# Kernel optimization log

Measured on AMD Instinct MI355X. Metric: run time of the kernel, lower is better.

## Reference

```python
import jax, jax.numpy as jnp
import numpy as np

N_NODES = 20000
N_EDGES = 320000
EMB = 256
K_DIFF = 3
BN_EPS = 1e-5


def conv1d(x, w, b, stride):
    # x: [N, Cin, L], w: [Cout, Cin, K]
    y = jax.lax.conv_general_dilated(x, w, window_strides=(stride,), padding='VALID',
                                     dimension_numbers=('NCH', 'OIH', 'NCH'))
    return y + b[None, :, None]


def batchnorm_train(x, gamma, beta):
    # training-mode BatchNorm1d over (N, L) per channel, biased variance
    m = jnp.mean(x, axis=(0, 2), keepdims=True)
    v = jnp.var(x, axis=(0, 2), keepdims=True)
    return (x - m) * jax.lax.rsqrt(v + BN_EPS) * gamma[None, :, None] + beta[None, :, None]


def dconv(X, W, b, row, col, norm_out, norm_in, n):
    # Diffusion convolution (pytorch_geometric_temporal DConv), K hops,
    # forward (out-degree) and backward (in-degree) random walks.
    def prop(x, norm):
        msg = norm[:, None] * x[row]                    # [E, F] gather
        return jax.ops.segment_sum(msg, col, num_segments=n)  # scatter-add to targets

    K = W.shape[1]
    Tx_0 = X
    Tx_1 = X
    H = X @ W[0, 0] + X @ W[1, 0]
    if K > 1:
        Tx_1_o = prop(X, norm_out)
        Tx_1_i = prop(X, norm_in)
        H = H + Tx_1_o @ W[0, 1] + Tx_1_i @ W[1, 1]
    for k in range(2, K):
        Tx_2_o = 2.0 * prop(Tx_1_o, norm_out) - Tx_0
        Tx_2_i = 2.0 * prop(Tx_1_i, norm_in) - Tx_0
        H = H + Tx_2_o @ W[0, k] + Tx_2_i @ W[1, k]
        Tx_0, Tx_1_o, Tx_1_i = Tx_1, Tx_2_o, Tx_2_i
    return H + b


def setup_inputs() -> dict:
    key = jax.random.key(0)
    ks = jax.random.split(key, 16)
    d_in = 2 * EMB  # concat([X, H])
    inp = {
        'x': jax.random.normal(ks[0], (N_NODES, 1, 100), dtype=jnp.float32),
        'edge_index': jax.random.randint(ks[1], (2, N_EDGES), 0, N_NODES, dtype=jnp.int32),
        'hidden_state': jax.random.normal(ks[2], (N_NODES, EMB), dtype=jnp.float32),
        'conv1_w': jax.random.normal(ks[3], (32, 1, 10), dtype=jnp.float32) * 0.2,
        'conv1_b': jnp.zeros((32,), jnp.float32),
        'bn1_gamma': jnp.ones((32,), jnp.float32),
        'bn1_beta': jnp.zeros((32,), jnp.float32),
        'conv2_w': jax.random.normal(ks[4], (32, 32, 10), dtype=jnp.float32) * 0.05,
        'conv2_b': jnp.zeros((32,), jnp.float32),
        'bn2_gamma': jnp.ones((32,), jnp.float32),
        'bn2_beta': jnp.zeros((32,), jnp.float32),
        'W_z': jax.random.normal(ks[5], (2, K_DIFF, d_in, EMB), dtype=jnp.float32) * 0.05,
        'b_z': jnp.zeros((EMB,), jnp.float32),
        'W_r': jax.random.normal(ks[6], (2, K_DIFF, d_in, EMB), dtype=jnp.float32) * 0.05,
        'b_r': jnp.zeros((EMB,), jnp.float32),
        'W_h': jax.random.normal(ks[7], (2, K_DIFF, d_in, EMB), dtype=jnp.float32) * 0.05,
        'b_h': jnp.zeros((EMB,), jnp.float32),
    }
    return inp


def reference(x, edge_index, hidden_state, conv1_w, conv1_b, bn1_gamma, bn1_beta,
              conv2_w, conv2_b, bn2_gamma, bn2_beta, W_z, b_z, W_r, b_r, W_h, b_h):
    n = x.shape[0]
    # CNN embedding: conv -> relu -> bn, twice
    h = batchnorm_train(jax.nn.relu(conv1d(x, conv1_w, conv1_b, 3)), bn1_gamma, bn1_beta)
    h = batchnorm_train(jax.nn.relu(conv1d(h, conv2_w, conv2_b, 3)), bn2_gamma, bn2_beta)
    X = h.reshape(n, -1)  # [N, EMB]

    row, col = edge_index[0], edge_index[1]
    ones = jnp.ones((row.shape[0],), X.dtype)
    deg_out = jax.ops.segment_sum(ones, row, num_segments=n)
    deg_in = jax.ops.segment_sum(ones, col, num_segments=n)
    norm_out = (1.0 / deg_out)[row]
    norm_in = (1.0 / deg_in)[col]

    H0 = hidden_state
    XH = jnp.concatenate([X, H0], axis=1)
    Z = jax.nn.sigmoid(dconv(XH, W_z, b_z, row, col, norm_out, norm_in, n))
    R = jax.nn.sigmoid(dconv(XH, W_r, b_r, row, col, norm_out, norm_in, n))
    XRH = jnp.concatenate([X, R * H0], axis=1)
    H_tilde = jnp.tanh(dconv(XRH, W_h, b_h, row, col, norm_out, norm_in, n))
    H = Z * H0 + (1.0 - Z) * H_tilde
    return jax.nn.relu(H)
```

## Files before the change

kernel.cpp:

```cpp
#include <hip/hip_runtime.h>
#include <cstdint>
#include <cstddef>

#define NN 20000
#define NE 320000
#define SBUF 10240000

typedef float f32x4 __attribute__((ext_vector_type(4)));
typedef short s16x8 __attribute__((ext_vector_type(8)));
typedef unsigned short us;

__device__ __forceinline__ us f2bf(float x){
    unsigned u = __float_as_uint(x);
    unsigned r = (u + 0x7fffu + ((u >> 16) & 1u)) >> 16;
    return (us)r;
}
__device__ __forceinline__ float bf2f(us s){
    return __uint_as_float(((unsigned)s) << 16);
}

__device__ __forceinline__ void gl16(const void* g, void* l){
    __builtin_amdgcn_global_load_lds((const __attribute__((address_space(1))) unsigned int*)g,
                                     (__attribute__((address_space(3))) unsigned int*)l, 16, 0, 0);
}

__device__ __forceinline__ void upd8(uint4 v, float w, float* ao, float* ai){
    float f0=__uint_as_float(v.x<<16), f1=__uint_as_float(v.x&0xffff0000u);
    float f2=__uint_as_float(v.y<<16), f3=__uint_as_float(v.y&0xffff0000u);
    float f4=__uint_as_float(v.z<<16), f5=__uint_as_float(v.z&0xffff0000u);
    float f6=__uint_as_float(v.w<<16), f7=__uint_as_float(v.w&0xffff0000u);
    ao[0]=fmaf(w,f0,ao[0]); ao[1]=fmaf(w,f1,ao[1]); ao[2]=fmaf(w,f2,ao[2]); ao[3]=fmaf(w,f3,ao[3]);
    ao[4]=fmaf(w,f4,ao[4]); ao[5]=fmaf(w,f5,ao[5]); ao[6]=fmaf(w,f6,ao[6]); ao[7]=fmaf(w,f7,ao[7]);
    ai[0]+=f0; ai[1]+=f1; ai[2]+=f2; ai[3]+=f3; ai[4]+=f4; ai[5]+=f5; ai[6]+=f6; ai[7]+=f7;
}
__device__ __forceinline__ void updw(uint4 v, float w, float* a){
    float f0=__uint_as_float(v.x<<16), f1=__uint_as_float(v.x&0xffff0000u);
    float f2=__uint_as_float(v.y<<16), f3=__uint_as_float(v.y&0xffff0000u);
    float f4=__uint_as_float(v.z<<16), f5=__uint_as_float(v.z&0xffff0000u);
    float f6=__uint_as_float(v.w<<16), f7=__uint_as_float(v.w&0xffff0000u);
    a[0]=fmaf(w,f0,a[0]); a[1]=fmaf(w,f1,a[1]); a[2]=fmaf(w,f2,a[2]); a[3]=fmaf(w,f3,a[3]);
    a[4]=fmaf(w,f4,a[4]); a[5]=fmaf(w,f5,a[5]); a[6]=fmaf(w,f6,a[6]); a[7]=fmaf(w,f7,a[7]);
}
__device__ __forceinline__ uint4 pack8(const float* a){
    uint4 r;
    r.x=((unsigned)f2bf(a[1])<<16)|f2bf(a[0]);
    r.y=((unsigned)f2bf(a[3])<<16)|f2bf(a[2]);
    r.z=((unsigned)f2bf(a[5])<<16)|f2bf(a[4]);
    r.w=((unsigned)f2bf(a[7])<<16)|f2bf(a[6]);
    return r;
}
__device__ __forceinline__ uint4 pack8s(const float* a, float s){
    uint4 r;
    r.x=((unsigned)f2bf(s*a[1])<<16)|f2bf(s*a[0]);
    r.y=((unsigned)f2bf(s*a[3])<<16)|f2bf(s*a[2]);
    r.z=((unsigned)f2bf(s*a[5])<<16)|f2bf(s*a[4]);
    r.w=((unsigned)f2bf(s*a[7])<<16)|f2bf(s*a[6]);
    return r;
}


__global__ void k_zero(uint32_t* p, int n){
    int i = blockIdx.x*256 + threadIdx.x;
    if(i < n) p[i] = 0u;
}

__global__ void k_degree(const int* __restrict__ ei, int* degout, int* degin){
    int e = blockIdx.x*256 + threadIdx.x;
    if(e < NE){
        atomicAdd(&degout[ei[e]], 1);
        atomicAdd(&degin[ei[NE+e]], 1);
    }
}

__global__ void k_scan(const int* __restrict__ degin, int* __restrict__ coloff,
                       float* __restrict__ invdegin){
    __shared__ int part[1024];
    int t = threadIdx.x;
    int base = t*20;
    int s = 0;
    for(int k=0;k<20;k++){ int i = base+k; if(i < NN) s += degin[i]; }
    part[t] = s;
    __syncthreads();
    for(int off=1; off<1024; off<<=1){
        int v = (t>=off) ? part[t-off] : 0;
        __syncthreads();
        part[t] += v;
        __syncthreads();
    }
    int run = (t>0) ? part[t-1] : 0;
    for(int k=0;k<20;k++){
        int i = base+k;
        if(i < NN){
            int d = degin[i];
            coloff[i] = run;
            run += d;
            invdegin[i] = (d>0) ? (1.0f/(float)d) : 0.0f;
        }
    }
    if(t==1023) coloff[NN] = part[1023];
}

__global__ void k_csr(const int* __restrict__ ei, const int* __restrict__ degout,
                      const int* __restrict__ coloff, int* cnt, int2* __restrict__ ew){
    int e = blockIdx.x*256 + threadIdx.x;
    if(e < NE){
        int r = ei[e], c = ei[NE+e];
        int pos = coloff[c] + atomicAdd(&cnt[c], 1);
        int2 v; v.x = r; v.y = __float_as_int(1.0f/(float)degout[r]);
        ew[pos] = v;
    }
}


__global__ void k_conv1(const float* __restrict__ x, const float* __restrict__ w1,
                        const float* __restrict__ b1, us* __restrict__ y1b){
    __shared__ float w[320];
    __shared__ float bb[32];
    int t = threadIdx.x;
    for(int i=t;i<320;i+=256) w[i] = w1[i];
    if(t < 32) bb[t] = b1[t];
    __syncthreads();
    int gid = blockIdx.x*256 + t;
    if(gid >= NN*31) return;
    int node = gid/31, p = gid - node*31;
    const float* xr = x + node*100 + 3*p;
    float xv[10];
    #pragma unroll
    for(int k=0;k<10;k++) xv[k] = xr[k];
    us* yo = y1b + (size_t)node*1024 + p;
    #pragma unroll
    for(int c=0;c<32;c++){
        float a = bb[c];
        #pragma unroll
        for(int k=0;k<10;k++) a = fmaf(w[c*10+k], xv[k], a);
        yo[c*32] = f2bf(fmaxf(a, 0.0f));
    }
    if(p == 0){
        #pragma unroll
        for(int c=0;c<32;c++) y1b[(size_t)node*1024 + c*32 + 31] = 0;
    }
}

template<int SLOTS, int PPC>
__global__ void k_chanstats_bf(const us* __restrict__ y, float* __restrict__ sq){
    int tid = blockIdx.x*blockDim.x + threadIdx.x;
    int slot = tid & (SLOTS-1);
    int node0 = tid / SLOTS;
    int nstride = (gridDim.x*blockDim.x) / SLOTS;
    int c = slot / PPC;
    float s = 0.f, q = 0.f;
    for(int n=node0; n<NN; n+=nstride){
        float v = bf2f(y[(size_t)n*SLOTS + slot]);
        s += v; q = fmaf(v, v, q);
    }
    #pragma unroll
    for(int m=PPC>>1; m>0; m>>=1){
        s += __shfl_xor(s, m);
        q += __shfl_xor(q, m);
    }
    if((threadIdx.x & (PPC-1)) == 0){
        atomicAdd(&sq[c], s);
        atomicAdd(&sq[32+c], q);
    }
}

__global__ void k_bnfin(const float* __restrict__ sq, const float* __restrict__ gamma,
                        const float* __restrict__ beta, float* __restrict__ scsh,
                        float inv_count){
    int c = threadIdx.x;
    if(c < 32){
        float m = sq[c]*inv_count;
        float v = sq[32+c]*inv_count - m*m;
        float sc = gamma[c]*rsqrtf(v + 1e-5f);
        scsh[c] = sc;
        scsh[32+c] = beta[c] - m*sc;
    }
}

__global__ void __launch_bounds__(256) k_conv2(const us* __restrict__ y1b,
                        const float* __restrict__ w2, const float* __restrict__ b2,
                        const float* __restrict__ scsh1, us* __restrict__ Xpre){
    __shared__ float wlds[10240];
    __shared__ float hlds[8*1040];
    int t = threadIdx.x;
    int node0 = blockIdx.x*8;
    #pragma unroll
    for(int j=0;j<40;j++){
        int idx = j*256 + t;
        int ck = idx>>5, c2 = idx&31;
        wlds[ck*32 + c2] = w2[c2*320 + ck];
    }
    #pragma unroll
    for(int j=0;j<32;j++){
        int idx = j*256 + t;
        int nl = idx>>10, i = idx&1023;
        int c = i>>5;
        hlds[nl*1040 + i] = fmaf(scsh1[c], bf2f(y1b[(size_t)(node0+nl)*1024 + i]), scsh1[32+c]);
    }
    __syncthreads();
    int nl = t>>5, c2 = t&31;
    int hbase = nl*1040;
    float acc[8];
    float b = b2[c2];
    #pragma unroll
    for(int p=0;p<8;p++) acc[p] = b;
    for(int c=0;c<32;c++){
        float wr[10];
        #pragma unroll
        for(int k=0;k<10;k++) wr[k] = wlds[(c*10+k)*32 + c2];
        float hv[32];
        #pragma unroll
        for(int q=0;q<8;q++){
            float4 v = *(const float4*)&hlds[hbase + c*32 + q*4];
            hv[q*4+0]=v.x; hv[q*4+1]=v.y; hv[q*4+2]=v.z; hv[q*4+3]=v.w;
        }
        #pragma unroll
        for(int p=0;p<8;p++){
            #pragma unroll
            for(int k=0;k<10;k++)
                acc[p] = fmaf(wr[k], hv[3*p+k], acc[p]);
        }
    }
    uint4 pk;
    pk.x = ((unsigned)f2bf(fmaxf(acc[1],0.f))<<16) | f2bf(fmaxf(acc[0],0.f));
    pk.y = ((unsigned)f2bf(fmaxf(acc[3],0.f))<<16) | f2bf(fmaxf(acc[2],0.f));
    pk.z = ((unsigned)f2bf(fmaxf(acc[5],0.f))<<16) | f2bf(fmaxf(acc[4],0.f));
    pk.w = ((unsigned)f2bf(fmaxf(acc[7],0.f))<<16) | f2bf(fmaxf(acc[6],0.f));
    *(uint4*)&Xpre[(size_t)(node0+nl)*256 + c2*8] = pk;
}

__global__ void __launch_bounds__(256) k_prep(const us* __restrict__ Xpre,
        const float* __restrict__ scsh, const float* __restrict__ h0,
        us* __restrict__ XHp){
    int node = blockIdx.x*4 + (threadIdx.x>>6);
    if(node >= NN) return;
    int lane = threadIdx.x & 63;
    int half = lane>>5, g = lane&31;
    uint4 o;
    if(half == 0){
        uint4 v = *(const uint4*)(Xpre + (size_t)node*256 + g*8);
        float sc = scsh[g], sh = scsh[32+g];
        float y[8];
        y[0]=fmaf(sc,__uint_as_float(v.x<<16),sh); y[1]=fmaf(sc,__uint_as_float(v.x&0xffff0000u),sh);
        y[2]=fmaf(sc,__uint_as_float(v.y<<16),sh); y[3]=fmaf(sc,__uint_as_float(v.y&0xffff0000u),sh);
        y[4]=fmaf(sc,__uint_as_float(v.z<<16),sh); y[5]=fmaf(sc,__uint_as_float(v.z&0xffff0000u),sh);
        y[6]=fmaf(sc,__uint_as_float(v.w<<16),sh); y[7]=fmaf(sc,__uint_as_float(v.w&0xffff0000u),sh);
        o = pack8(y);
    }else{
        float4 a = *(const float4*)(h0 + (size_t)node*256 + g*8);
        float4 b = *(const float4*)(h0 + (size_t)node*256 + g*8 + 4);
        float y[8] = {a.x,a.y,a.z,a.w,b.x,b.y,b.z,b.w};
        o = pack8(y);
    }
    *(uint4*)(XHp + (size_t)node*512 + (size_t)g*16 + half*8) = o;
}


__device__ __forceinline__ float weff_val(const float* W, int term, size_t base){
    const size_t S = 512*256;
    if(term==0)      return W[0*S+base] + W[3*S+base] - W[2*S+base] - W[5*S+base];
    else if(term==1) return W[1*S+base];
    else if(term==2) return W[4*S+base];
    else if(term==3) return 2.0f*W[2*S+base];
    else             return 2.0f*W[5*S+base];
}

__global__ void k_weff_zr_t(const float* __restrict__ Wz, const float* __restrict__ Wr,
                            us* __restrict__ Wt){
    int k = blockIdx.x*256 + threadIdx.x;
    int col = blockIdx.y;
    const float* W = (col < 256) ? Wz : Wr;
    int j = col & 255;
    int kb = k >> 8, rr = k & 255;
    size_t base = (size_t)((kb & 1)*256 + rr)*256 + j;
    Wt[(size_t)col*2560 + k] = f2bf(weff_val(W, kb>>1, base));
}

__global__ void k_weff_h_t(const float* __restrict__ Wh, us* __restrict__ Wt){
    int k = blockIdx.x*256 + threadIdx.x;
    int col = blockIdx.y;
    int kb = k >> 8, rr = k & 255;
    size_t base = (size_t)((kb & 1)*256 + rr)*256 + col;
    Wt[(size_t)col*2560 + k] = f2bf(weff_val(Wh, kb>>1, base));
}


__global__ void __launch_bounds__(256) k_prop1(const us* __restrict__ XHp,
        const int* __restrict__ coloff, const int2* __restrict__ ew,
        const float* __restrict__ invdeg, us* __restrict__ T1op, us* __restrict__ T1ip){
    int node = blockIdx.x*4 + (threadIdx.x>>6);
    if(node >= NN) return;
    int lane = threadIdx.x & 63;
    size_t lo = (size_t)(lane&31)*16 + (lane>>5)*8;
    int s = coloff[node], e = coloff[node+1];
    float ao[8]={0,0,0,0,0,0,0,0}, ai[8]={0,0,0,0,0,0,0,0};
    int j = s;
    for(; j+7 < e; j += 8){
        int2 ed[8]; uint4 v[8];
        #pragma unroll
        for(int i=0;i<8;i++) ed[i] = ew[j+i];
        #pragma unroll
        for(int i=0;i<8;i++) v[i] = *(const uint4*)(XHp+(size_t)ed[i].x*512+lo);
        #pragma unroll
        for(int i=0;i<8;i++) upd8(v[i], __int_as_float(ed[i].y), ao, ai);
    }
    for(; j < e; j++){
        int2 ed = ew[j];
        uint4 v = *(const uint4*)(XHp+(size_t)ed.x*512+lo);
        upd8(v, __int_as_float(ed.y), ao, ai);
    }
    float wi = invdeg[node];
    *(uint4*)(T1op+(size_t)node*512+lo) = pack8(ao);
    *(uint4*)(T1ip+(size_t)node*512+lo) = pack8s(ai,wi);
}

__global__ void __launch_bounds__(256) k_prop2(const us* __restrict__ T1op,
        const us* __restrict__ T1ip,
        const int* __restrict__ coloff, const int2* __restrict__ ew,
        const float* __restrict__ invdeg, us* __restrict__ P2op, us* __restrict__ P2ip){
    int node = blockIdx.x*4 + (threadIdx.x>>6);
    if(node >= NN) return;
    int lane = threadIdx.x & 63;
    size_t lo = (size_t)(lane&31)*16 + (lane>>5)*8;
    int s = coloff[node], e = coloff[node+1];
    float ao[8]={0,0,0,0,0,0,0,0}, ai[8]={0,0,0,0,0,0,0,0};
    int j = s;
    for(; j+3 < e; j += 4){
        int2 ed[4]; uint4 va[4], vb[4];
        #pragma unroll
        for(int i=0;i<4;i++) ed[i] = ew[j+i];
        #pragma unroll
        for(int i=0;i<4;i++){
            size_t o = (size_t)ed[i].x*512+lo;
            va[i] = *(const uint4*)(T1op+o);
            vb[i] = *(const uint4*)(T1ip+o);
        }
        #pragma unroll
        for(int i=0;i<4;i++){
            updw(va[i], __int_as_float(ed[i].y), ao);
            updw(vb[i], 1.0f, ai);
        }
    }
    for(; j < e; j++){
        int2 ed = ew[j];
        size_t o = (size_t)ed.x*512+lo;
        updw(*(const uint4*)(T1op+o), __int_as_float(ed.y), ao);
        updw(*(const uint4*)(T1ip+o), 1.0f, ai);
    }
    float wi = invdeg[node];
    *(uint4*)(P2op+(size_t)node*512+lo) = pack8(ao);
    *(uint4*)(P2ip+(size_t)node*512+lo) = pack8s(ai,wi);
}

__global__ void __launch_bounds__(256) k_propu(const us* __restrict__ Yin,
        const int* __restrict__ coloff, const int2* __restrict__ ew,
        const float* __restrict__ invdeg, us* __restrict__ Pout){
    int node = blockIdx.x*4 + (threadIdx.x>>6);
    if(node >= NN) return;
    int lane = threadIdx.x & 63;
    int half = lane>>5;
    size_t lo = (size_t)(lane&31)*16 + half*8;
    int s = coloff[node], e = coloff[node+1];
    float a[8]={0,0,0,0,0,0,0,0};
    int j = s;
    for(; j+7 < e; j += 8){
        int2 ed[8]; uint4 v[8];
        #pragma unroll
        for(int i=0;i<8;i++) ed[i] = ew[j+i];
        #pragma unroll
        for(int i=0;i<8;i++) v[i] = *(const uint4*)(Yin+(size_t)ed[i].x*512+lo);
        #pragma unroll
        for(int i=0;i<8;i++) updw(v[i], half ? 1.0f : __int_as_float(ed[i].y), a);
    }
    for(; j < e; j++){
        int2 ed = ew[j];
        uint4 v = *(const uint4*)(Yin+(size_t)ed.x*512+lo);
        updw(v, half ? 1.0f : __int_as_float(ed.y), a);
    }
    float sc = half ? invdeg[node] : 1.0f;
    *(uint4*)(Pout+(size_t)node*512+lo) = pack8s(a,sc);
}


template<int MODE, int BNT>
__global__ void __launch_bounds__(256) k_gemm(const us* __restrict__ XG,
        const us* __restrict__ RG, const us* __restrict__ Wt,
        const float* __restrict__ bias0, const float* __restrict__ bias1,
        const float* __restrict__ h0, const float* __restrict__ Zin,
        float* __restrict__ out0, us* __restrict__ out1){
    constexpr int WN = BNT/32;
    constexpr int NB = BNT/64;
    __shared__ us As[2][4096];
    __shared__ us Bs[2][BNT*32];
    int t = threadIdx.x;
    int wid = t >> 6, lane = t & 63;
    int l15 = lane & 15, kg = lane >> 4;

    int bid = blockIdx.x;
    int xcd = bid & 7, sblk = bid >> 3;
    int cidx = sblk & 3, r = (sblk >> 2)*8 + xcd;
    if(r >= 157) return;
    int row0 = r*128, col0 = cidx*BNT;
    int rowbase = (wid >> 1)*64, colbase = (wid & 1)*(BNT/2);
    int swz = (l15 >> 1) & 3;

    int srA[2], sgA[2];
    size_t rowoffA[2];
    #pragma unroll
    for(int i=0;i<2;i++){
        int c = t + i*256;
        srA[i] = c >> 2;
        sgA[i] = (c & 3) ^ ((srA[i] >> 1) & 3);
        int gr = row0 + srA[i];
        gr = (gr < NN) ? gr : NN-1;
        rowoffA[i] = (size_t)gr*512 + (size_t)sgA[i]*16;
    }
    int srB[NB], sgB[NB];
    size_t coloffB[NB];
    #pragma unroll
    for(int i=0;i<NB;i++){
        int c = t + i*256;
        srB[i] = c >> 2;
        sgB[i] = (c & 3) ^ ((srB[i] >> 1) & 3);
        coloffB[i] = (size_t)(col0+srB[i])*2560 + (size_t)sgB[i]*8;
    }

    f32x4 acc[4][WN] = {};

    auto stage = [&](int buf, int s){
        int kb = s >> 3;
        int ktc = (s & 7) * 4;
        const us* Ap;
        if(MODE == 0){
            Ap = XG + (size_t)(kb >> 1) * SBUF + (size_t)(kb & 1) * 8;
        }else{
            if((kb & 1) == 0) Ap = XG + (size_t)(kb >> 1) * SBUF;
            else Ap = RG + (size_t)((kb + 1) >> 2) * SBUF + (size_t)(((kb + 1) >> 1) & 1) * 8;
        }
        #pragma unroll
        for(int i=0;i<2;i++)
            gl16(Ap + rowoffA[i] + (size_t)ktc*16, &As[buf][(t+i*256)*8]);
        const us* Wp = Wt + (size_t)kb*256 + (s & 7)*32;
        #pragma unroll
        for(int i=0;i<NB;i++)
            gl16(Wp + coloffB[i], &Bs[buf][(t+i*256)*8]);
    };

    stage(0, 0);
    stage(1, 1);
    for(int step=0; step<80; ++step){
        int cur = step & 1;
        if(step < 79){
            if(MODE == 0) asm volatile("s_waitcnt vmcnt(4)" ::: "memory");
            else          asm volatile("s_waitcnt vmcnt(3)" ::: "memory");
        }else{
            asm volatile("s_waitcnt vmcnt(0)" ::: "memory");
        }
        __builtin_amdgcn_s_barrier();
        s16x8 af[4], bfr[WN];
        #pragma unroll
        for(int i=0;i<4;i++){
            int row = rowbase + i*16 + l15;
            af[i] = *(const s16x8*)&As[cur][(row*4 + (kg ^ swz))*8];
        }
        #pragma unroll
        for(int n=0;n<WN;n++){
            int colr = colbase + n*16 + l15;
            bfr[n] = *(const s16x8*)&Bs[cur][(colr*4 + (kg ^ swz))*8];
        }
        asm volatile("s_waitcnt lgkmcnt(0)" ::: "memory");
        __builtin_amdgcn_sched_barrier(0);
        __builtin_amdgcn_s_barrier();
        if(step < 78) stage(cur, step+2);
        __builtin_amdgcn_s_setprio(1);
        #pragma unroll
        for(int mi=0;mi<4;mi++){
            #pragma unroll
            for(int ni=0;ni<WN;ni++){
                acc[mi][ni] = __builtin_amdgcn_mfma_f32_16x16x32_bf16(
                    af[mi], bfr[ni], acc[mi][ni], 0, 0, 0);
            }
        }
        __builtin_amdgcn_s_setprio(0);
    }

    #pragma unroll
    for(int mi=0;mi<4;mi++){
        int gr0 = row0 + rowbase + mi*16 + kg*4;
        #pragma unroll
        for(int ni=0;ni<WN;ni++){
            int j = col0 + colbase + ni*16 + l15;
            #pragma unroll
            for(int rr=0;rr<4;rr++){
                int gr = gr0 + rr;
                if(gr < NN){
                    float a = acc[mi][ni][rr];
                    if(MODE == 0){
                        if(j < 256){
                            out0[(size_t)gr*256 + j] = 1.0f/(1.0f + expf(-(a + bias0[j])));
                        }else{
                            int jj = j - 256;
                            float rv = 1.0f/(1.0f + expf(-(a + bias1[jj])));
                            us v = f2bf(rv * h0[(size_t)gr*256 + jj]);
                            size_t base = (size_t)gr*512 + (size_t)(jj>>3)*16 + (jj&7);
                            out1[base] = v;
                            out1[base+8] = v;
                        }
                    }else{
                        float z = Zin[(size_t)gr*256 + j];
                        float ht = tanhf(a + bias0[j]);
                        float H = z*h0[(size_t)gr*256 + j] + (1.0f - z)*ht;
                        out0[(size_t)gr*256 + j] = fmaxf(H, 0.0f);
                    }
                }
            }
        }
    }
}


extern "C" void kernel_launch(void* const* d_in, const int* in_sizes, int n_in,
                              void* d_out, int out_size, void* d_ws, size_t ws_size,
                              hipStream_t stream){
    const float* x   = (const float*)d_in[0];
    const int*   ei  = (const int*)  d_in[1];
    const float* h0  = (const float*)d_in[2];
    const float* w1  = (const float*)d_in[3];
    const float* b1  = (const float*)d_in[4];
    const float* g1  = (const float*)d_in[5];
    const float* be1 = (const float*)d_in[6];
    const float* w2  = (const float*)d_in[7];
    const float* b2  = (const float*)d_in[8];
    const float* g2  = (const float*)d_in[9];
    const float* be2 = (const float*)d_in[10];
    const float* Wz  = (const float*)d_in[11];
    const float* bz  = (const float*)d_in[12];
    const float* Wr  = (const float*)d_in[13];
    const float* br  = (const float*)d_in[14];
    const float* Wh  = (const float*)d_in[15];
    const float* bh  = (const float*)d_in[16];
    float* out = (float*)d_out;
    float* wsf = (float*)d_ws;
    (void)in_sizes; (void)n_in; (void)out_size;

    const size_t O_DEGO=0, O_DEGI=20000, O_CNT=40000, O_BN=60000;
    const size_t O_COLOFF=60288, O_EW=80384, O_INVDEG=720384;
    const size_t O_WTZR=740480, O_WTH=1395840;
    const size_t O_XPRE=1723520;
    const size_t O_XG=4283520;
    const size_t O_RG=29883520;
    const size_t O_Z=45243520;
    const size_t WS_NEED_BYTES = (size_t)50363520 * 4;
    if(ws_size < WS_NEED_BYTES) return;

    const size_t SW = 5120000;

    int* degout = (int*)(wsf + O_DEGO);
    int* degin  = (int*)(wsf + O_DEGI);
    int* cnt    = (int*)(wsf + O_CNT);
    float* bn   = wsf + O_BN;
    int* coloff = (int*)(wsf + O_COLOFF);
    int2* ew    = (int2*)(wsf + O_EW);
    float* invdeg = wsf + O_INVDEG;
    us* Wtzr = (us*)(wsf + O_WTZR);
    us* Wth  = (us*)(wsf + O_WTH);
    us* Xpre = (us*)(wsf + O_XPRE);
    us* XG   = (us*)(wsf + O_XG);
    us* RG   = (us*)(wsf + O_RG);
    us* XHp  = XG;
    us* T1op = (us*)(wsf + O_XG + SW);
    us* T1ip = (us*)(wsf + O_XG + 2*SW);
    us* P2op = (us*)(wsf + O_XG + 3*SW);
    us* P2ip = (us*)(wsf + O_XG + 4*SW);
    us* RHp  = RG;
    us* Q1p  = (us*)(wsf + O_RG + SW);
    us* Q2p  = (us*)(wsf + O_RG + 2*SW);
    float* Z = wsf + O_Z;
    us* y1b  = T1op;

    k_zero<<<236,256,0,stream>>>((uint32_t*)(wsf + O_DEGO), 60256);
    k_degree<<<1250,256,0,stream>>>(ei, degout, degin);
    k_scan<<<1,1024,0,stream>>>(degin, coloff, invdeg);
    k_csr<<<1250,256,0,stream>>>(ei, degout, coloff, cnt, ew);

    k_conv1<<<2422,256,0,stream>>>(x, w1, b1, y1b);
    k_chanstats_bf<1024,32><<<256,256,0,stream>>>(y1b, bn+0);
    k_bnfin<<<1,32,0,stream>>>(bn+0, g1, be1, bn+64, 1.0f/620000.0f);
    k_conv2<<<2500,256,0,stream>>>(y1b, w2, b2, bn+64, Xpre);
    k_chanstats_bf<256,8><<<64,256,0,stream>>>(Xpre, bn+128);
    k_bnfin<<<1,32,0,stream>>>(bn+128, g2, be2, bn+192, 1.0f/160000.0f);
    k_prep<<<5000,256,0,stream>>>(Xpre, bn+192, h0, XHp);

    k_weff_zr_t<<<dim3(10,512),256,0,stream>>>(Wz, Wr, Wtzr);
    k_weff_h_t<<<dim3(10,256),256,0,stream>>>(Wh, Wth);

    k_prop1<<<5000,256,0,stream>>>(XHp, coloff, ew, invdeg, T1op, T1ip);
    k_prop2<<<5000,256,0,stream>>>(T1op, T1ip, coloff, ew, invdeg, P2op, P2ip);

    k_gemm<0,128><<<640,256,0,stream>>>(XG, RG, Wtzr, bz, br, h0, nullptr, Z, RHp);

    k_propu<<<5000,256,0,stream>>>(RHp, coloff, ew, invdeg, Q1p);
    k_propu<<<5000,256,0,stream>>>(Q1p, coloff, ew, invdeg, Q2p);

    k_gemm<1,64><<<640,256,0,stream>>>(XG, RG, Wth, bh, nullptr, h0, Z, out, nullptr);
}
```

Baseline: 793.0 us.

## Rewrite conv2 as bf16 MFMA GEMM with BN1 folded into weights

conv1 now writes its output transposed (position-major, channel-contiguous) so that conv2 can be expressed as an im2col GEMM. conv2 runs on 16x16x32 bf16 MFMA instructions, replacing the scalar FMA loop over LDS. The BN1 scale is folded into bf16 weights and the BN1 shift into a per-channel bias by two small new kernels. The prop kernels also use readfirstlane on the CSR offsets to keep the loop bounds scalar. Rounding the folded weights to bf16 adds some precision loss compared with the fp32 path.

```diff
diff --git a/kernel.cpp b/kernel.cpp
--- a/kernel.cpp
+++ b/kernel.cpp
@@ -113,7 +113,7 @@
 
 
 __global__ void k_conv1(const float* __restrict__ x, const float* __restrict__ w1,
-                        const float* __restrict__ b1, us* __restrict__ y1b){
+                        const float* __restrict__ b1, us* __restrict__ y1T){
     __shared__ float w[320];
     __shared__ float bb[32];
     int t = threadIdx.x;
@@ -121,23 +121,47 @@
     if(t < 32) bb[t] = b1[t];
     __syncthreads();
     int gid = blockIdx.x*256 + t;
-    if(gid >= NN*31) return;
-    int node = gid/31, p = gid - node*31;
+    int node = gid>>5, p = gid&31;
+    us* yo = y1T + (size_t)node*1024 + p*32;
+    if(p >= 31){
+        uint4 z = {0,0,0,0};
+        *(uint4*)yo = z; *(uint4*)(yo+8) = z;
+        *(uint4*)(yo+16) = z; *(uint4*)(yo+24) = z;
+        return;
+    }
     const float* xr = x + node*100 + 3*p;
     float xv[10];
     #pragma unroll
     for(int k=0;k<10;k++) xv[k] = xr[k];
-    us* yo = y1b + (size_t)node*1024 + p;
+    float o[32];
     #pragma unroll
     for(int c=0;c<32;c++){
         float a = bb[c];
         #pragma unroll
         for(int k=0;k<10;k++) a = fmaf(w[c*10+k], xv[k], a);
-        yo[c*32] = f2bf(fmaxf(a, 0.0f));
-    }
-    if(p == 0){
-        #pragma unroll
-        for(int c=0;c<32;c++) y1b[(size_t)node*1024 + c*32 + 31] = 0;
+        o[c] = fmaxf(a, 0.0f);
+    }
+    *(uint4*)yo      = pack8(o);
+    *(uint4*)(yo+8)  = pack8(o+8);
+    *(uint4*)(yo+16) = pack8(o+16);
+    *(uint4*)(yo+24) = pack8(o+24);
+}
+
+__global__ void k_chanstats_T(const us* __restrict__ y, float* __restrict__ sq){
+    int tid = blockIdx.x*256 + threadIdx.x;
+    int slot = tid & 1023;
+    int c = slot & 31;
+    int node0 = tid >> 10;
+    float s = 0.f, q = 0.f;
+    for(int n=node0; n<NN; n+=64){
+        float v = bf2f(y[(size_t)n*1024 + slot]);
+        s += v; q = fmaf(v, v, q);
+    }
+    s += __shfl_xor(s, 32);
+    q += __shfl_xor(q, 32);
+    if((threadIdx.x & 63) < 32){
+        atomicAdd(&sq[c], s);
+        atomicAdd(&sq[32+c], q);
     }
 }
 
@@ -177,56 +201,59 @@
     }
 }
 
-__global__ void __launch_bounds__(256) k_conv2(const us* __restrict__ y1b,
-                        const float* __restrict__ w2, const float* __restrict__ b2,
-                        const float* __restrict__ scsh1, us* __restrict__ Xpre){
-    __shared__ float wlds[10240];
-    __shared__ float hlds[8*1040];
+__global__ void k_wfold(const float* __restrict__ w2, const float* __restrict__ scsh1,
+                        us* __restrict__ Bf){
+    int idx = blockIdx.x*256 + threadIdx.x;
+    if(idx >= 10240) return;
+    int kk = idx >> 10, c2 = (idx >> 5) & 31, c = idx & 31;
+    Bf[idx] = f2bf(scsh1[c] * w2[c2*320 + c*10 + kk]);
+}
+
+__global__ void k_wbias(const float* __restrict__ w2, const float* __restrict__ scsh1,
+                        const float* __restrict__ b2, float* __restrict__ biasc){
     int t = threadIdx.x;
-    int node0 = blockIdx.x*8;
-    #pragma unroll
-    for(int j=0;j<40;j++){
-        int idx = j*256 + t;
-        int ck = idx>>5, c2 = idx&31;
-        wlds[ck*32 + c2] = w2[c2*320 + ck];
-    }
-    #pragma unroll
-    for(int j=0;j<32;j++){
-        int idx = j*256 + t;
-        int nl = idx>>10, i = idx&1023;
-        int c = i>>5;
-        hlds[nl*1040 + i] = fmaf(scsh1[c], bf2f(y1b[(size_t)(node0+nl)*1024 + i]), scsh1[32+c]);
-    }
-    __syncthreads();
-    int nl = t>>5, c2 = t&31;
-    int hbase = nl*1040;
-    float acc[8];
-    float b = b2[c2];
-    #pragma unroll
-    for(int p=0;p<8;p++) acc[p] = b;
-    for(int c=0;c<32;c++){
-        float wr[10];
-        #pragma unroll
-        for(int k=0;k<10;k++) wr[k] = wlds[(c*10+k)*32 + c2];
-        float hv[32];
-        #pragma unroll
-        for(int q=0;q<8;q++){
-            float4 v = *(const float4*)&hlds[hbase + c*32 + q*4];
-            hv[q*4+0]=v.x; hv[q*4+1]=v.y; hv[q*4+2]=v.z; hv[q*4+3]=v.w;
-        }
-        #pragma unroll
-        for(int p=0;p<8;p++){
-            #pragma unroll
-            for(int k=0;k<10;k++)
-                acc[p] = fmaf(wr[k], hv[3*p+k], acc[p]);
-        }
-    }
-    uint4 pk;
-    pk.x = ((unsigned)f2bf(fmaxf(acc[1],0.f))<<16) | f2bf(fmaxf(acc[0],0.f));
-    pk.y = ((unsigned)f2bf(fmaxf(acc[3],0.f))<<16) | f2bf(fmaxf(acc[2],0.f));
-    pk.z = ((unsigned)f2bf(fmaxf(acc[5],0.f))<<16) | f2bf(fmaxf(acc[4],0.f));
-    pk.w = ((unsigned)f2bf(fmaxf(acc[7],0.f))<<16) | f2bf(fmaxf(acc[6],0.f));
-    *(uint4*)&Xpre[(size_t)(node0+nl)*256 + c2*8] = pk;
+    int c2 = t >> 3, part = t & 7;
+    float s = 0.f;
+    for(int i=part; i<320; i+=8)
+        s += scsh1[32 + i/10] * w2[c2*320 + i];
+    s += __shfl_xor(s,1); s += __shfl_xor(s,2); s += __shfl_xor(s,4);
+    if(part == 0) biasc[c2] = b2[c2] + s;
+}
+
+__global__ void __launch_bounds__(256) k_conv2m(const us* __restrict__ y1T,
+        const us* __restrict__ Bf, const float* __restrict__ biasc,
+        us* __restrict__ Xpre){
+    int t = threadIdx.x;
+    int wv = t>>6, l = t&63;
+    int l15 = l&15, g = l>>4;
+    int r0 = blockIdx.x*64 + wv*16;
+    int arow = r0 + l15;
+    int an = arow>>3, ap = arow&7;
+    const us* abase = y1T + (size_t)an*1024 + (3*ap)*32 + g*8;
+    const us* bbase = Bf + (size_t)l15*32 + g*8;
+    f32x4 acc0 = {}, acc1 = {};
+    #pragma unroll
+    for(int kk=0;kk<10;kk++){
+        s16x8 af = *(const s16x8*)(abase + kk*32);
+        s16x8 b0 = *(const s16x8*)(bbase + kk*1024);
+        s16x8 b1 = *(const s16x8*)(bbase + kk*1024 + 512);
+        acc0 = __builtin_amdgcn_mfma_f32_16x16x32_bf16(af, b0, acc0, 0, 0, 0);
+        acc1 = __builtin_amdgcn_mfma_f32_16x16x32_bf16(af, b1, acc1, 0, 0, 0);
+    }
+    int base = r0 + g*4;
+    int n = base>>3, p0 = base&7;
+    #pragma unroll
+    for(int nf=0;nf<2;nf++){
+        int c2 = nf*16 + l15;
+        float bb = biasc[c2];
+        f32x4 a = nf ? acc1 : acc0;
+        float v0 = fmaxf(a[0]+bb,0.f), v1 = fmaxf(a[1]+bb,0.f);
+        float v2 = fmaxf(a[2]+bb,0.f), v3 = fmaxf(a[3]+bb,0.f);
+        uint2 pk;
+        pk.x = ((unsigned)f2bf(v1)<<16)|f2bf(v0);
+        pk.y = ((unsigned)f2bf(v3)<<16)|f2bf(v2);
+        *(uint2*)&Xpre[(size_t)n*256 + c2*8 + p0] = pk;
+    }
 }
 
 __global__ void __launch_bounds__(256) k_prep(const us* __restrict__ Xpre,
@@ -292,7 +319,8 @@
     if(node >= NN) return;
     int lane = threadIdx.x & 63;
     size_t lo = (size_t)(lane&31)*16 + (lane>>5)*8;
-    int s = coloff[node], e = coloff[node+1];
+    int s = __builtin_amdgcn_readfirstlane(coloff[node]);
+    int e = __builtin_amdgcn_readfirstlane(coloff[node+1]);
     float ao[8]={0,0,0,0,0,0,0,0}, ai[8]={0,0,0,0,0,0,0,0};
     int j = s;
     for(; j+7 < e; j += 8){
@@ -322,7 +350,8 @@
     if(node >= NN) return;
     int lane = threadIdx.x & 63;
     size_t lo = (size_t)(lane&31)*16 + (lane>>5)*8;
-    int s = coloff[node], e = coloff[node+1];
+    int s = __builtin_amdgcn_readfirstlane(coloff[node]);
+    int e = __builtin_amdgcn_readfirstlane(coloff[node+1]);
     float ao[8]={0,0,0,0,0,0,0,0}, ai[8]={0,0,0,0,0,0,0,0};
     int j = s;
     for(; j+3 < e; j += 4){
@@ -360,7 +389,8 @@
     int lane = threadIdx.x & 63;
     int half = lane>>5;
     size_t lo = (size_t)(lane&31)*16 + half*8;
-    int s = coloff[node], e = coloff[node+1];
+    int s = __builtin_amdgcn_readfirstlane(coloff[node]);
+    int e = __builtin_amdgcn_readfirstlane(coloff[node+1]);
     float a[8]={0,0,0,0,0,0,0,0};
     int j = s;
     for(; j+7 < e; j += 8){
@@ -550,7 +580,8 @@
     const size_t O_XG=4283520;
     const size_t O_RG=29883520;
     const size_t O_Z=45243520;
-    const size_t WS_NEED_BYTES = (size_t)50363520 * 4;
+    const size_t O_BF=50363520;
+    const size_t WS_NEED_BYTES = (size_t)50366080 * 4;
     if(ws_size < WS_NEED_BYTES) return;
 
     const size_t SW = 5120000;
@@ -576,17 +607,20 @@
     us* Q1p  = (us*)(wsf + O_RG + SW);
     us* Q2p  = (us*)(wsf + O_RG + 2*SW);
     float* Z = wsf + O_Z;
-    us* y1b  = T1op;
+    us* Bf   = (us*)(wsf + O_BF);
+    us* y1T  = T1op;
 
     k_zero<<<236,256,0,stream>>>((uint32_t*)(wsf + O_DEGO), 60256);
     k_degree<<<1250,256,0,stream>>>(ei, degout, degin);
     k_scan<<<1,1024,0,stream>>>(degin, coloff, invdeg);
     k_csr<<<1250,256,0,stream>>>(ei, degout, coloff, cnt, ew);
 
-    k_conv1<<<2422,256,0,stream>>>(x, w1, b1, y1b);
-    k_chanstats_bf<1024,32><<<256,256,0,stream>>>(y1b, bn+0);
+    k_conv1<<<2500,256,0,stream>>>(x, w1, b1, y1T);
+    k_chanstats_T<<<256,256,0,stream>>>(y1T, bn+0);
     k_bnfin<<<1,32,0,stream>>>(bn+0, g1, be1, bn+64, 1.0f/620000.0f);
-    k_conv2<<<2500,256,0,stream>>>(y1b, w2, b2, bn+64, Xpre);
+    k_wfold<<<40,256,0,stream>>>(w2, bn+64, Bf);
+    k_wbias<<<1,256,0,stream>>>(w2, bn+64, b2, bn+256);
+    k_conv2m<<<2500,256,0,stream>>>(y1T, Bf, bn+256, Xpre);
     k_chanstats_bf<256,8><<<64,256,0,stream>>>(Xpre, bn+128);
     k_bnfin<<<1,32,0,stream>>>(bn+128, g2, be2, bn+192, 1.0f/160000.0f);
     k_prep<<<5000,256,0,stream>>>(Xpre, bn+192, h0, XHp);
```

Measured after the change: 732.1 us. 7.7% less time.
